# Performance work log

Measured on AMD Instinct MI355X. Metric: run time of the kernel, lower is better.

The kernel has to match this reference:

```python
import jax, jax.numpy as jnp
import numpy as np
from jax import lax


def setup_inputs() -> dict:
    key = jax.random.key(0)
    B, S, C = 64, 4096, 128
    timeseries = jax.random.normal(key, (B, S, C), dtype=jnp.float32)
    return {"timeseries": timeseries, "k": 64}


def reference(timeseries, k):
    B, S, C = timeseries.shape
    ffts = jnp.fft.rfft(timeseries, axis=1)          # (B, F, C) complex, F = S//2 + 1
    F = ffts.shape[1]
    mags = jnp.abs(ffts)                              # (B, F, C)
    # top-k magnitudes per (batch, channel): move freq axis last for lax.top_k
    m = jnp.transpose(mags, (0, 2, 1))                # (B, C, F)
    _, idx = lax.top_k(m, k)                          # (B, C, k)
    mask = jnp.zeros((B, C, F), dtype=bool)
    mask = mask.at[jnp.arange(B)[:, None, None],
                   jnp.arange(C)[None, :, None],
                   idx].set(True)
    mask = jnp.transpose(mask, (0, 2, 1))             # (B, F, C)
    filtered = jnp.where(mask, ffts, jnp.zeros((), dtype=ffts.dtype))
    reconstructed = jnp.fft.irfft(filtered, n=S, axis=1)  # (B, S, C) real
    return reconstructed.astype(timeseries.dtype)
```

## Files before the change

### kernel.cpp

```cpp
#include <hip/hip_runtime.h>
#include <math.h>

#define TPB 256
#define SWZ(i) ((i) ^ (((i) >> 5) & 31) ^ ((i) >> 10))

#define A2048 0.0030679615757712823f
#define A256  0.0245436926061702596f
#define A32   0.1963495408493620774f
#define APACK 0.0015339807878856411f
#define EPSB  1.220703125e-4f

__device__ __forceinline__ float2 cadd(float2 a, float2 b){return make_float2(a.x+b.x, a.y+b.y);}
__device__ __forceinline__ float2 csub(float2 a, float2 b){return make_float2(a.x-b.x, a.y-b.y);}
__device__ __forceinline__ float2 cmul(float2 a, float2 b){return make_float2(a.x*b.x-a.y*b.y, a.x*b.y+a.y*b.x);}
__device__ __forceinline__ float2 cni(float2 a){return make_float2(a.y, -a.x);}
__device__ __forceinline__ float2 cpi(float2 a){return make_float2(-a.y, a.x);}

__device__ __forceinline__ int pos2048(int k) {
  return 256*(k&7) + 32*((k>>3)&7) + 4*((k>>6)&7) + ((k>>9)&3);
}

__device__ __forceinline__ void fft8(float2 y[8]) {
  const float S2 = 0.70710678118654752f;
  float2 B0=cadd(y[0],y[4]), B4=csub(y[0],y[4]);
  float2 B1=cadd(y[1],y[5]), B5=csub(y[1],y[5]);
  float2 B2=cadd(y[2],y[6]), B6=csub(y[2],y[6]);
  float2 B3=cadd(y[3],y[7]), B7=csub(y[3],y[7]);
  float2 C0=cadd(B0,B2), C2=csub(B0,B2);
  float2 C1=cadd(B1,B3), C3=csub(B1,B3);
  float2 n6=cni(B6), n7=cni(B7);
  float2 C4=cadd(B4,n6), C6=csub(B4,n6);
  float2 C5=cadd(B5,n7), C7=csub(B5,n7);
  y[0]=cadd(C0,C1); y[4]=csub(C0,C1);
  float2 n3=cni(C3);
  y[2]=cadd(C2,n3); y[6]=csub(C2,n3);
  float2 t5=make_float2(S2*(C5.x+C5.y), S2*(C5.y-C5.x));
  y[1]=cadd(C4,t5); y[5]=csub(C4,t5);
  float2 t7=make_float2(S2*(C7.y-C7.x), -S2*(C7.x+C7.y));
  y[3]=cadd(C6,t7); y[7]=csub(C6,t7);
}

__device__ __forceinline__ void ifft8(float2 y[8]) {
  const float S2 = 0.70710678118654752f;
  float2 B0=cadd(y[0],y[4]), B4=csub(y[0],y[4]);
  float2 B1=cadd(y[1],y[5]), B5=csub(y[1],y[5]);
  float2 B2=cadd(y[2],y[6]), B6=csub(y[2],y[6]);
  float2 B3=cadd(y[3],y[7]), B7=csub(y[3],y[7]);
  float2 C0=cadd(B0,B2), C2=csub(B0,B2);
  float2 C1=cadd(B1,B3), C3=csub(B1,B3);
  float2 p6=cpi(B6), p7=cpi(B7);
  float2 C4=cadd(B4,p6), C6=csub(B4,p6);
  float2 C5=cadd(B5,p7), C7=csub(B5,p7);
  y[0]=cadd(C0,C1); y[4]=csub(C0,C1);
  float2 p3=cpi(C3);
  y[2]=cadd(C2,p3); y[6]=csub(C2,p3);
  float2 t5=make_float2(S2*(C5.x-C5.y), S2*(C5.x+C5.y));
  y[1]=cadd(C4,t5); y[5]=csub(C4,t5);
  float2 t7=make_float2(-S2*(C7.x+C7.y), S2*(C7.x-C7.y));
  y[3]=cadd(C6,t7); y[7]=csub(C6,t7);
}

__device__ __forceinline__ void r8stage(float2* Zf, int idx0, int st, float a1, bool inv) {
  float2 y[8];
#pragma unroll
  for (int s=0;s<8;++s) y[s]=Zf[SWZ(idx0+st*s)];
  float sn, cs; __sincosf(a1, &sn, &cs);
  float2 w1=make_float2(cs,sn);
  float2 w2=cmul(w1,w1), w3=cmul(w2,w1), w4=cmul(w2,w2);
  float2 w5=cmul(w4,w1), w6=cmul(w4,w2), w7=cmul(w4,w3);
  if (inv){
    y[1]=cmul(y[1],w1); y[2]=cmul(y[2],w2); y[3]=cmul(y[3],w3);
    y[4]=cmul(y[4],w4); y[5]=cmul(y[5],w5); y[6]=cmul(y[6],w6); y[7]=cmul(y[7],w7);
    ifft8(y);
  } else {
    fft8(y);
    y[1]=cmul(y[1],w1); y[2]=cmul(y[2],w2); y[3]=cmul(y[3],w3);
    y[4]=cmul(y[4],w4); y[5]=cmul(y[5],w5); y[6]=cmul(y[6],w6); y[7]=cmul(y[7],w7);
  }
#pragma unroll
  for (int s=0;s<8;++s) Zf[SWZ(idx0+st*s)] = y[s];
}

__global__ __launch_bounds__(256) void tposeV(const float* __restrict__ in,
                                              float* __restrict__ out,
                                              int R, int Cd) {
  __shared__ float tile[64][65];
  int t = threadIdx.x;
  int q = t & 15, r = t >> 4;
  int b = blockIdx.z;
  int c0 = blockIdx.x * 64, r0 = blockIdx.y * 64;
  const float4* in4 = reinterpret_cast<const float4*>(in + (size_t)b * R * Cd);
  float4* out4 = reinterpret_cast<float4*>(out + (size_t)b * R * Cd);
#pragma unroll
  for (int rr = r; rr < 64; rr += 16) {
    float4 v = in4[((size_t)(r0 + rr) * Cd + c0) / 4 + q];
    tile[rr][4 * q + 0] = v.x; tile[rr][4 * q + 1] = v.y;
    tile[rr][4 * q + 2] = v.z; tile[rr][4 * q + 3] = v.w;
  }
  __syncthreads();
#pragma unroll
  for (int cc = r; cc < 64; cc += 16) {
    float4 w;
    w.x = tile[4 * q + 0][cc]; w.y = tile[4 * q + 1][cc];
    w.z = tile[4 * q + 2][cc]; w.w = tile[4 * q + 3][cc];
    out4[((size_t)(c0 + cc) * R + r0) / 4 + q] = w;
  }
}

__global__ __launch_bounds__(TPB, 4) void fourier_topk_kernel(
    const float* __restrict__ src, float* __restrict__ dst,
    const int* __restrict__ kptr, int strideT) {
  __shared__ float2 Zf[2048];
  __shared__ float keyF[2049];
  __shared__ unsigned int hist[256];
  __shared__ unsigned char maskA[2052];
  __shared__ int tieIdx[64];
  __shared__ double candV[64];
  __shared__ double cpR[4], cpI[4];
  __shared__ unsigned int bcD, bcR, bcCnt, bcT, bcG, bcTieN;

  const int tid = threadIdx.x;
  int i = blockIdx.x;
  int xj = i & 7, mm = i >> 3;
  int c = 16 * xj + (mm & 15);
  int b = mm >> 4;
  const size_t base = (strideT == 1) ? ((size_t)(b * 128 + c)) * 4096
                                     : ((size_t)b * 4096 * 128 + (size_t)c);
  const float* sp = src + base;
  float* dp = dst + base;

  if (strideT == 1) {
    const float4* sp4 = reinterpret_cast<const float4*>(sp);
#pragma unroll
    for (int it = 0; it < 4; ++it) {
      int t4 = tid + 256 * it;
      float4 v = sp4[t4];
      Zf[SWZ(2*t4)]   = make_float2(v.x, v.y);
      Zf[SWZ(2*t4+1)] = make_float2(v.z, v.w);
    }
  } else {
#pragma unroll
    for (int it = 0; it < 8; ++it) {
      int n = tid + 256 * it;
      float a = sp[(size_t)(2*n) * strideT];
      float bb = sp[(size_t)(2*n+1) * strideT];
      Zf[SWZ(n)] = make_float2(a, bb);
    }
  }
  __syncthreads();

  r8stage(Zf, tid, 256, -A2048 * (float)tid, false);
  __syncthreads();
  r8stage(Zf, 256*(tid>>5) + (tid&31), 32, -A256 * (float)(tid&31), false);
  __syncthreads();
  r8stage(Zf, 32*(tid>>2) + (tid&3), 4, -A32 * (float)(tid&3), false);
  __syncthreads();
#pragma unroll
  for (int h = 0; h < 2; ++h) {
    int i0 = 4 * (tid + 256*h);
    float2 A0=Zf[SWZ(i0)], A1=Zf[SWZ(i0+1)], A2=Zf[SWZ(i0+2)], A3=Zf[SWZ(i0+3)];
    float2 f=cadd(A0,A2), e=csub(A0,A2), g=cadd(A1,A3), d=csub(A1,A3);
    float2 nd=cni(d);
    Zf[SWZ(i0)]   = cadd(f,g);
    Zf[SWZ(i0+1)] = cadd(e,nd);
    Zf[SWZ(i0+2)] = csub(f,g);
    Zf[SWZ(i0+3)] = csub(e,nd);
  }
  __syncthreads();

#pragma unroll
  for (int jj = 0; jj < 4; ++jj) {
    int k = tid + 256 * jj;
    float2 za = Zf[SWZ(pos2048(k))];
    float2 zb = Zf[SWZ(pos2048((2048 - k) & 2047))];
    float her = 0.5f*(za.x+zb.x), hei = 0.5f*(za.y-zb.y);
    float hor = 0.5f*(za.y+zb.y), hoi = -0.5f*(za.x-zb.x);
    float sn, cs; __sincosf(-APACK * (float)k, &sn, &cs);
    float whr = cs*hor - sn*hoi, whi = cs*hoi + sn*hor;
    float x1r = her + whr, x1i = hei + whi;
    float x2r = her - whr, x2i = whi - hei;
    keyF[k]        = x1r*x1r + x1i*x1i;
    keyF[2048 - k] = x2r*x2r + x2i*x2i;
  }
  if (tid == 0) {
    float2 za = Zf[SWZ(pos2048(1024))];
    keyF[1024] = za.x*za.x + za.y*za.y;
  }
  __syncthreads();

  int kk = kptr[0];
  if (kk > 2049) kk = 2049;
  if (kk < 1) kk = 1;
  unsigned int prefix = 0u, pmask = 0u, Tkey = 0u;
  bool haveT = false;
  int R = kk;
#pragma unroll 1
  for (int p = 0; p < 4; ++p) {
    if (!haveT) {
      const int sh = 24 - 8 * p;
      hist[tid] = 0u;
      __syncthreads();
      for (int k = tid; k <= 2048; k += TPB) {
        unsigned int u = __float_as_uint(keyF[k]);
        if ((u & pmask) == prefix) atomicAdd(&hist[(u >> sh) & 255u], 1u);
      }
      __syncthreads();
      if (tid < 64) {
        int L = tid;
        int s0 = (int)hist[4*L], s1 = (int)hist[4*L+1];
        int s2 = (int)hist[4*L+2], s3 = (int)hist[4*L+3];
        int loc = s0 + s1 + s2 + s3;
        int suf = loc;
#pragma unroll
        for (int off = 1; off < 64; off <<= 1) {
          int t = __shfl(suf, (L + off) & 63, 64);
          suf += (L + off < 64) ? t : 0;
        }
        int e3 = suf - loc, i3 = e3 + s3;
        int e2 = i3,        i2 = e2 + s2;
        int e1 = i2,        i1 = e1 + s1;
        int e0 = i1,        i0 = e0 + s0;
        if (e3 < R && R <= i3) { bcD = 4*L+3; bcR = R - e3; bcCnt = s3; }
        if (e2 < R && R <= i2) { bcD = 4*L+2; bcR = R - e2; bcCnt = s2; }
        if (e1 < R && R <= i1) { bcD = 4*L+1; bcR = R - e1; bcCnt = s1; }
        if (e0 < R && R <= i0) { bcD = 4*L+0; bcR = R - e0; bcCnt = s0; }
      }
      __syncthreads();
      prefix |= (bcD << sh);
      pmask |= (255u << sh);
      R = (int)bcR;
      if (bcCnt == 1u) {
        for (int k = tid; k <= 2048; k += TPB) {
          unsigned int u = __float_as_uint(keyF[k]);
          if ((u & pmask) == prefix) bcT = u;
        }
        __syncthreads();
        Tkey = bcT;
        haveT = true;
      }
      __syncthreads();
    }
  }
  if (!haveT) Tkey = prefix;

  float Tf = __uint_as_float(Tkey);
  float Thi = Tf * (1.0f + EPSB), Tlo = Tf * (1.0f - EPSB);
  if (tid == 0) { bcG = 0u; bcTieN = 0u; }
  __syncthreads();
  for (int k = tid; k <= 2048; k += TPB) {
    float v = keyF[k];
    if (v > Thi) atomicAdd(&bcG, 1u);
    else if (v >= Tlo) {
      int pos = (int)atomicAdd(&bcTieN, 1u);
      if (pos < 64) tieIdx[pos] = k;
    }
  }
  __syncthreads();
  int G = (int)bcG, E = (int)bcTieN, need = kk - G;

  if (need >= E) {
    for (int k = tid; k <= 2048; k += TPB)
      maskA[k] = (keyF[k] >= Tlo) ? 1 : 0;
    __syncthreads();
  } else {
    for (int k = tid; k <= 2048; k += TPB)
      maskA[k] = (keyF[k] > Thi) ? 1 : 0;
    __syncthreads();
    int nt = E < 64 ? E : 64;
    for (int ci = 0; ci < nt; ++ci) {
      int kq = tieIdx[ci];
      double sr = 0.0, si = 0.0;
#pragma unroll 1
      for (int j = 0; j < 16; ++j) {
        int m = tid + 256 * j;
        double xm = (double)sp[(size_t)m * strideT];
        int a = (kq * m) & 4095;
        double ang = 1.5339807878856412e-3 * (double)a;
        double sv, cv; sincos(ang, &sv, &cv);
        sr += xm * cv; si -= xm * sv;
      }
#pragma unroll
      for (int off = 1; off < 64; off <<= 1) {
        sr += __shfl_xor(sr, off); si += __shfl_xor(si, off);
      }
      if ((tid & 63) == 0) { cpR[tid >> 6] = sr; cpI[tid >> 6] = si; }
      __syncthreads();
      if (tid == 0) {
        double Rr = cpR[0]+cpR[1]+cpR[2]+cpR[3];
        double Ii = cpI[0]+cpI[1]+cpI[2]+cpI[3];
        candV[ci] = Rr*Rr + Ii*Ii;
      }
      __syncthreads();
    }
    if (tid == 0) {
      unsigned char* ch = (unsigned char*)hist;
      for (int t = 0; t < nt; ++t) ch[t] = 0;
      int lim = need < nt ? need : nt;
      for (int s = 0; s < lim; ++s) {
        int best = -1;
        for (int t = 0; t < nt; ++t) {
          if (ch[t]) continue;
          if (best < 0 || candV[t] > candV[best] ||
              (candV[t] == candV[best] && tieIdx[t] < tieIdx[best])) best = t;
        }
        if (best >= 0) { ch[best] = 1; maskA[tieIdx[best]] = 1; }
      }
    }
    __syncthreads();
  }

#pragma unroll
  for (int jj = 0; jj < 4; ++jj) {
    int k = tid + 256 * jj;
    if (k == 0) {
      int p0 = SWZ(pos2048(0));
      float2 z0 = Zf[p0];
      float X0 = z0.x + z0.y, XN = z0.x - z0.y;
      float A = maskA[0] ? X0 : 0.0f, Bv = maskA[2048] ? XN : 0.0f;
      Zf[p0] = make_float2(0.5f*(A + Bv), 0.5f*(A - Bv));
      int p1 = SWZ(pos2048(1024));
      float2 z1 = Zf[p1];
      float m1 = maskA[1024] ? 1.0f : 0.0f;
      Zf[p1] = make_float2(m1 * z1.x, m1 * z1.y);
    } else {
      int pa = SWZ(pos2048(k)), pb = SWZ(pos2048(2048 - k));
      float2 za = Zf[pa], zb = Zf[pb];
      float her = 0.5f*(za.x+zb.x), hei = 0.5f*(za.y-zb.y);
      float hor = 0.5f*(za.y+zb.y), hoi = -0.5f*(za.x-zb.x);
      float sn, cs; __sincosf(-APACK * (float)k, &sn, &cs);
      float wr = cs, wi = sn;
      float whr = wr*hor - wi*hoi, whi = wr*hoi + wi*hor;
      float x1r = her + whr, x1i = hei + whi;
      float x2r = her - whr, x2i = whi - hei;
      float mA = maskA[k] ? 1.0f : 0.0f, mB = maskA[2048 - k] ? 1.0f : 0.0f;
      float Ar = mA*x1r, Ai = mA*x1i, Br = mB*x2r, Bi = mB*x2i;
      float sr = Ar + Br, si = Ai - Bi;
      float dr = Ar - Br, di = Ai + Bi;
      float tr = wr*dr + wi*di, ti = wr*di - wi*dr;
      Zf[pa] = make_float2(0.5f*(sr - ti), 0.5f*(si + tr));
      Zf[pb] = make_float2(0.5f*(sr + ti), 0.5f*(tr - si));
    }
  }
  __syncthreads();

#pragma unroll
  for (int h = 0; h < 2; ++h) {
    int i0 = 4 * (tid + 256*h);
    float2 y0=Zf[SWZ(i0)], y1=Zf[SWZ(i0+1)], y2=Zf[SWZ(i0+2)], y3=Zf[SWZ(i0+3)];
    float2 f=cadd(y0,y2), e=csub(y0,y2), g=cadd(y1,y3), d=csub(y1,y3);
    float2 pd=cpi(d);
    Zf[SWZ(i0)]   = cadd(f,g);
    Zf[SWZ(i0+1)] = cadd(e,pd);
    Zf[SWZ(i0+2)] = csub(f,g);
    Zf[SWZ(i0+3)] = csub(e,pd);
  }
  __syncthreads();
  r8stage(Zf, 32*(tid>>2) + (tid&3), 4, A32 * (float)(tid&3), true);
  __syncthreads();
  r8stage(Zf, 256*(tid>>5) + (tid&31), 32, A256 * (float)(tid&31), true);
  __syncthreads();
  r8stage(Zf, tid, 256, A2048 * (float)tid, true);
  __syncthreads();

  const float scf = 1.0f / 2048.0f;
  if (strideT == 1) {
    float4* dp4 = reinterpret_cast<float4*>(dp);
#pragma unroll
    for (int it = 0; it < 4; ++it) {
      int t4 = tid + 256 * it;
      float2 v0 = Zf[SWZ(2*t4)], v1 = Zf[SWZ(2*t4+1)];
      dp4[t4] = make_float4(v0.x*scf, v0.y*scf, v1.x*scf, v1.y*scf);
    }
  } else {
#pragma unroll
    for (int it = 0; it < 8; ++it) {
      int n = tid + 256 * it;
      float2 v = Zf[SWZ(n)];
      dp[(size_t)(2*n) * strideT]   = v.x * scf;
      dp[(size_t)(2*n+1) * strideT] = v.y * scf;
    }
  }
}

extern "C" void kernel_launch(void* const* d_in, const int* in_sizes, int n_in,
                              void* d_out, int out_size, void* d_ws, size_t ws_size,
                              hipStream_t stream) {
  (void)in_sizes; (void)n_in; (void)out_size;
  const float* ts = (const float*)d_in[0];
  const int* kptr = (const int*)d_in[1];
  float* out = (float*)d_out;
  float* ws = (float*)d_ws;
  const int B = 64, S = 4096, C = 128;
  const size_t sigBytes = (size_t)B * S * C * sizeof(float);

  if (ws_size >= sigBytes) {
    tposeV<<<dim3(C / 64, S / 64, B), 256, 0, stream>>>(ts, ws, S, C);
    fourier_topk_kernel<<<B * C, TPB, 0, stream>>>(ws, ws, kptr, 1);
    tposeV<<<dim3(S / 64, C / 64, B), 256, 0, stream>>>(ws, out, C, S);
  } else {
    fourier_topk_kernel<<<B * C, TPB, 0, stream>>>(ts, out, kptr, C);
  }
}
```

Measured before the change: 432.5 us.

## Keep spectrum keys in registers, per-wave histograms, remap transpose blocks

Power-spectrum keys are now kept in per-thread registers rather than a shared keyF array. Radix-select histograms are split into four per-wavefront copies to reduce atomic contention, and the launch-bounds occupancy hint is raised from 4 to 6 blocks. The transpose kernels use a 1D grid with a swizzled block-to-tile mapping, likely to spread memory channel or XCD traffic. Freeing LDS should allow more resident blocks, at the cost of more registers and a bigger histogram to clear and sum each pass.

```diff
diff --git a/kernel.cpp b/kernel.cpp
--- a/kernel.cpp
+++ b/kernel.cpp
@@ -81,14 +81,19 @@
   for (int s=0;s<8;++s) Zf[SWZ(idx0+st*s)] = y[s];
 }
 
-__global__ __launch_bounds__(256) void tposeV(const float* __restrict__ in,
+__global__ __launch_bounds__(256) void tposeX(const float* __restrict__ in,
                                               float* __restrict__ out,
-                                              int R, int Cd) {
+                                              int R, int Cd, int lgx) {
   __shared__ float tile[64][65];
   int t = threadIdx.x;
   int q = t & 15, r = t >> 4;
-  int b = blockIdx.z;
-  int c0 = blockIdx.x * 64, r0 = blockIdx.y * 64;
+  int id = blockIdx.x;
+  int g = id & 7, j = id >> 3;
+  int w = ((j >> 3) << 6) | (g << 3) | (j & 7);
+  int b = w >> 7;
+  int rem = w & 127;
+  int gxm = (1 << lgx) - 1;
+  int c0 = (rem & gxm) * 64, r0 = (rem >> lgx) * 64;
   const float4* in4 = reinterpret_cast<const float4*>(in + (size_t)b * R * Cd);
   float4* out4 = reinterpret_cast<float4*>(out + (size_t)b * R * Cd);
 #pragma unroll
@@ -100,19 +105,18 @@
   __syncthreads();
 #pragma unroll
   for (int cc = r; cc < 64; cc += 16) {
-    float4 w;
-    w.x = tile[4 * q + 0][cc]; w.y = tile[4 * q + 1][cc];
-    w.z = tile[4 * q + 2][cc]; w.w = tile[4 * q + 3][cc];
-    out4[((size_t)(c0 + cc) * R + r0) / 4 + q] = w;
-  }
-}
-
-__global__ __launch_bounds__(TPB, 4) void fourier_topk_kernel(
+    float4 wv;
+    wv.x = tile[4 * q + 0][cc]; wv.y = tile[4 * q + 1][cc];
+    wv.z = tile[4 * q + 2][cc]; wv.w = tile[4 * q + 3][cc];
+    out4[((size_t)(c0 + cc) * R + r0) / 4 + q] = wv;
+  }
+}
+
+__global__ __launch_bounds__(TPB, 6) void fourier_topk_kernel(
     const float* __restrict__ src, float* __restrict__ dst,
     const int* __restrict__ kptr, int strideT) {
   __shared__ float2 Zf[2048];
-  __shared__ float keyF[2049];
-  __shared__ unsigned int hist[256];
+  __shared__ unsigned int histL[1056];
   __shared__ unsigned char maskA[2052];
   __shared__ int tieIdx[64];
   __shared__ double candV[64];
@@ -168,6 +172,7 @@
   }
   __syncthreads();
 
+  float kA[4], kB[4];
 #pragma unroll
   for (int jj = 0; jj < 4; ++jj) {
     int k = tid + 256 * jj;
@@ -179,14 +184,15 @@
     float whr = cs*hor - sn*hoi, whi = cs*hoi + sn*hor;
     float x1r = her + whr, x1i = hei + whi;
     float x2r = her - whr, x2i = whi - hei;
-    keyF[k]        = x1r*x1r + x1i*x1i;
-    keyF[2048 - k] = x2r*x2r + x2i*x2i;
-  }
-  if (tid == 0) {
+    kA[jj] = x1r*x1r + x1i*x1i;
+    kB[jj] = x2r*x2r + x2i*x2i;
+  }
+  float kNy;
+  {
     float2 za = Zf[SWZ(pos2048(1024))];
-    keyF[1024] = za.x*za.x + za.y*za.y;
-  }
-  __syncthreads();
+    kNy = za.x*za.x + za.y*za.y;
+  }
+  const bool hasNy = (tid == 0);
 
   int kk = kptr[0];
   if (kk > 2049) kk = 2049;
@@ -194,27 +200,40 @@
   unsigned int prefix = 0u, pmask = 0u, Tkey = 0u;
   bool haveT = false;
   int R = kk;
+  unsigned int* myh = &histL[(tid >> 6) * 264];
 #pragma unroll 1
   for (int p = 0; p < 4; ++p) {
     if (!haveT) {
       const int sh = 24 - 8 * p;
-      hist[tid] = 0u;
-      __syncthreads();
-      for (int k = tid; k <= 2048; k += TPB) {
-        unsigned int u = __float_as_uint(keyF[k]);
-        if ((u & pmask) == prefix) atomicAdd(&hist[(u >> sh) & 255u], 1u);
+      for (int idx2 = tid; idx2 < 1056; idx2 += TPB) histL[idx2] = 0u;
+      __syncthreads();
+#pragma unroll
+      for (int jj = 0; jj < 4; ++jj) {
+        unsigned int u = __float_as_uint(kA[jj]);
+        if ((u & pmask) == prefix) atomicAdd(&myh[(u >> sh) & 255u], 1u);
+        u = __float_as_uint(kB[jj]);
+        if ((u & pmask) == prefix) atomicAdd(&myh[(u >> sh) & 255u], 1u);
+      }
+      if (hasNy) {
+        unsigned int u = __float_as_uint(kNy);
+        if ((u & pmask) == prefix) atomicAdd(&myh[(u >> sh) & 255u], 1u);
       }
       __syncthreads();
       if (tid < 64) {
         int L = tid;
-        int s0 = (int)hist[4*L], s1 = (int)hist[4*L+1];
-        int s2 = (int)hist[4*L+2], s3 = (int)hist[4*L+3];
+        int s0 = 0, s1 = 0, s2 = 0, s3 = 0;
+#pragma unroll
+        for (int wv = 0; wv < 4; ++wv) {
+          const unsigned int* hw = &histL[wv * 264];
+          s0 += (int)hw[4*L]; s1 += (int)hw[4*L+1];
+          s2 += (int)hw[4*L+2]; s3 += (int)hw[4*L+3];
+        }
         int loc = s0 + s1 + s2 + s3;
         int suf = loc;
 #pragma unroll
         for (int off = 1; off < 64; off <<= 1) {
-          int t = __shfl(suf, (L + off) & 63, 64);
-          suf += (L + off < 64) ? t : 0;
+          int tt = __shfl(suf, (L + off) & 63, 64);
+          suf += (L + off < 64) ? tt : 0;
         }
         int e3 = suf - loc, i3 = e3 + s3;
         int e2 = i3,        i2 = e2 + s2;
@@ -230,8 +249,15 @@
       pmask |= (255u << sh);
       R = (int)bcR;
       if (bcCnt == 1u) {
-        for (int k = tid; k <= 2048; k += TPB) {
-          unsigned int u = __float_as_uint(keyF[k]);
+#pragma unroll
+        for (int jj = 0; jj < 4; ++jj) {
+          unsigned int u = __float_as_uint(kA[jj]);
+          if ((u & pmask) == prefix) bcT = u;
+          u = __float_as_uint(kB[jj]);
+          if ((u & pmask) == prefix) bcT = u;
+        }
+        if (hasNy) {
+          unsigned int u = __float_as_uint(kNy);
           if ((u & pmask) == prefix) bcT = u;
         }
         __syncthreads();
@@ -247,24 +273,48 @@
   float Thi = Tf * (1.0f + EPSB), Tlo = Tf * (1.0f - EPSB);
   if (tid == 0) { bcG = 0u; bcTieN = 0u; }
   __syncthreads();
-  for (int k = tid; k <= 2048; k += TPB) {
-    float v = keyF[k];
+#pragma unroll
+  for (int jj = 0; jj < 4; ++jj) {
+    float v = kA[jj];
     if (v > Thi) atomicAdd(&bcG, 1u);
     else if (v >= Tlo) {
       int pos = (int)atomicAdd(&bcTieN, 1u);
-      if (pos < 64) tieIdx[pos] = k;
+      if (pos < 64) tieIdx[pos] = tid + 256 * jj;
+    }
+    v = kB[jj];
+    if (v > Thi) atomicAdd(&bcG, 1u);
+    else if (v >= Tlo) {
+      int pos = (int)atomicAdd(&bcTieN, 1u);
+      if (pos < 64) tieIdx[pos] = 2048 - (tid + 256 * jj);
+    }
+  }
+  if (hasNy) {
+    if (kNy > Thi) atomicAdd(&bcG, 1u);
+    else if (kNy >= Tlo) {
+      int pos = (int)atomicAdd(&bcTieN, 1u);
+      if (pos < 64) tieIdx[pos] = 1024;
     }
   }
   __syncthreads();
   int G = (int)bcG, E = (int)bcTieN, need = kk - G;
 
   if (need >= E) {
-    for (int k = tid; k <= 2048; k += TPB)
-      maskA[k] = (keyF[k] >= Tlo) ? 1 : 0;
+#pragma unroll
+    for (int jj = 0; jj < 4; ++jj) {
+      int k = tid + 256 * jj;
+      maskA[k]        = (kA[jj] >= Tlo) ? 1 : 0;
+      maskA[2048 - k] = (kB[jj] >= Tlo) ? 1 : 0;
+    }
+    if (hasNy) maskA[1024] = (kNy >= Tlo) ? 1 : 0;
     __syncthreads();
   } else {
-    for (int k = tid; k <= 2048; k += TPB)
-      maskA[k] = (keyF[k] > Thi) ? 1 : 0;
+#pragma unroll
+    for (int jj = 0; jj < 4; ++jj) {
+      int k = tid + 256 * jj;
+      maskA[k]        = (kA[jj] > Thi) ? 1 : 0;
+      maskA[2048 - k] = (kB[jj] > Thi) ? 1 : 0;
+    }
+    if (hasNy) maskA[1024] = (kNy > Thi) ? 1 : 0;
     __syncthreads();
     int nt = E < 64 ? E : 64;
     for (int ci = 0; ci < nt; ++ci) {
@@ -293,7 +343,7 @@
       __syncthreads();
     }
     if (tid == 0) {
-      unsigned char* ch = (unsigned char*)hist;
+      unsigned char* ch = (unsigned char*)histL;
       for (int t = 0; t < nt; ++t) ch[t] = 0;
       int lim = need < nt ? need : nt;
       for (int s = 0; s < lim; ++s) {
@@ -394,9 +444,9 @@
   const size_t sigBytes = (size_t)B * S * C * sizeof(float);
 
   if (ws_size >= sigBytes) {
-    tposeV<<<dim3(C / 64, S / 64, B), 256, 0, stream>>>(ts, ws, S, C);
+    tposeX<<<8192, 256, 0, stream>>>(ts, ws, S, C, 1);
     fourier_topk_kernel<<<B * C, TPB, 0, stream>>>(ws, ws, kptr, 1);
-    tposeV<<<dim3(S / 64, C / 64, B), 256, 0, stream>>>(ws, out, C, S);
+    tposeX<<<8192, 256, 0, stream>>>(ws, out, C, S, 6);
   } else {
     fourier_topk_kernel<<<B * C, TPB, 0, stream>>>(ts, out, kptr, C);
   }
```

New measurement: 437.6 us. Within noise of the previous version (+1.2%).
